# Kernel optimization log

Measured on AMD Instinct MI355X. Metric: run time of the kernel, lower is better.

The kernel has to match this reference:

```python
import jax, jax.numpy as jnp
import numpy as np

N_HEADS = 8
NUM_CLASSES = 8
ATTN_INTENSE = 1.0


def setup_inputs() -> dict:
    key = jax.random.key(0)
    k1, k2, k3, k4 = jax.random.split(key, 4)
    bs, width, T = 8, 1536, 1024
    qkv = jax.random.normal(k1, (bs, width, T), dtype=jnp.float32)
    attn_mask = jax.random.randint(k2, (bs, 32, 32), 0, NUM_CLASSES, dtype=jnp.int32)
    # class embedding table: NUM_CLASSES rows + 1 null row (used for the global pass)
    embed_table = jax.random.normal(k3, (NUM_CLASSES + 1, 512), dtype=jnp.float32) * 0.02
    # Conv1d(embed_dim=512 -> 3*ch=192, kernel=1, bias=False) weight
    W_cls = jax.random.normal(k4, (192, 512), dtype=jnp.float32) * 0.02
    return {"qkv": qkv, "attn_mask": attn_mask, "embed_table": embed_table, "W_cls": W_cls}


def _attend(q, k, v, scale):
    # q,k,v: [B, T, C]; returns [B, T, C]
    logits = jnp.einsum('btc,bsc->bts', q * scale, k * scale)
    w = jax.nn.softmax(logits, axis=-1)
    return jnp.einsum('bts,bsc->btc', w, v)


def reference(qkv, attn_mask, embed_table, W_cls):
    bs, width, T = qkv.shape
    H = N_HEADS
    ch = width // (3 * H)            # 64
    scale = ch ** -0.25              # 1/sqrt(sqrt(ch))
    bH = bs * H

    qkv_h = qkv.reshape(bH, 3 * ch, T)
    q = jnp.transpose(qkv_h[:, 0 * ch:1 * ch], (0, 2, 1))  # [bH, T, ch]
    k = jnp.transpose(qkv_h[:, 1 * ch:2 * ch], (0, 2, 1))
    v = jnp.transpose(qkv_h[:, 2 * ch:3 * ch], (0, 2, 1))

    # ---- global pass with null class token ----
    null_tok = W_cls @ embed_table[NUM_CLASSES]  # [3*ch]
    qn, kn, vn = null_tok[:ch], null_tok[ch:2 * ch], null_tok[2 * ch:]
    a = _attend(q + qn, k + kn, v + vn, scale)   # [bH, T, ch]

    # ---- per-region (per segmentation class) attention ----
    seg = attn_mask.reshape(bs, T)
    segs = jnp.repeat(seg, H, axis=0)            # [bH, T], sample-major like qkv reshape

    out = a
    counter = jnp.ones((bH, T), dtype=qkv.dtype)
    for c in range(NUM_CLASSES):
        tok = W_cls @ embed_table[c]             # [3*ch], same token at every region position
        qc, kc, vc = tok[:ch], tok[ch:2 * ch], tok[2 * ch:]
        m = segs == c                            # [bH, T]
        logits = jnp.einsum('btc,bsc->bts', (q + qc) * scale, (k + kc) * scale)
        logits = jnp.where(m[:, None, :], logits, -1e9)   # restrict keys to region
        w = jax.nn.softmax(logits, axis=-1)
        a_c = jnp.einsum('bts,bsc->btc', w, v + vc)
        out = out + jnp.where(m[:, :, None], a_c, 0.0)    # scatter-add onto region queries
        counter = counter + ATTN_INTENSE * m.astype(counter.dtype)

    out = out / counter[:, :, None]              # [bH, T, ch]
    # faithful to original: outs are [ch, T] each, torch.stack(dim=1) -> [ch, bH, T], then reshape
    stacked = jnp.transpose(out, (2, 0, 1))      # [ch, bH, T]
    return stacked.reshape(bs, H * ch, T)
```

## Files before the change

kernel.cpp:

```cpp
#include <hip/hip_runtime.h>
#include <stdint.h>

typedef unsigned short u16;
typedef unsigned int   u32;
typedef __bf16 bf16_t;
typedef bf16_t bf16x8 __attribute__((ext_vector_type(8)));
typedef bf16_t bf16x2 __attribute__((ext_vector_type(2)));
typedef float  f32x2  __attribute__((ext_vector_type(2)));
typedef float  f32x4  __attribute__((ext_vector_type(4)));

#define QSCALE 0.18033688011112042f

__device__ __forceinline__ u32 pkbf(float a, float b) {
  f32x2 x = {a, b};
  bf16x2 y = __builtin_convertvector(x, bf16x2);
  union { bf16x2 v; u32 u; } c; c.v = y; return c.u;
}

__device__ __forceinline__ float fexp2(float x) {
#if __has_builtin(__builtin_amdgcn_exp2f)
  return __builtin_amdgcn_exp2f(x);
#else
  float r;
  asm("v_exp_f32 %0, %1\n\ts_nop 0" : "=v"(r) : "v"(x));
  return r;
#endif
}

__device__ __forceinline__ void gload_lds16(const void* g, void* l) {
  __builtin_amdgcn_global_load_lds(
      (const __attribute__((address_space(1))) void*)g,
      (__attribute__((address_space(3))) void*)l, 16, 0, 0);
}

__global__ __launch_bounds__(256)
void prep_kernel(const float* __restrict__ qkv,
                 const float* __restrict__ W, const float* __restrict__ E,
                 float* __restrict__ tok, u16* __restrict__ tiles) {
  const int B = blockIdx.x;
  const int tid = threadIdx.x;
  if (B >= 1024) {
    const int gw = (B - 1024) * 4 + (tid >> 6);
    const int lane = tid & 63;
    if (gw < 1728) {
      const int c = gw / 192, j = gw - c * 192;
      const f32x4* w4 = (const f32x4*)(W + (size_t)j * 512 + lane * 8);
      const f32x4* e4 = (const f32x4*)(E + (size_t)c * 512 + lane * 8);
      float acc = 0.f;
#pragma unroll
      for (int i = 0; i < 2; ++i) {
        f32x4 w = w4[i], e = e4[i];
        acc += w.x * e.x + w.y * e.y + w.z * e.z + w.w * e.w;
      }
#pragma unroll
      for (int off = 32; off; off >>= 1) acc += __shfl_xor(acc, off, 64);
      if (lane == 0) tok[c * 192 + j] = acc;
    }
    return;
  }
  const int bh = B >> 4, kt = B & 15;
  const int s0 = kt * 64;
  const float* qg = qkv + (size_t)bh * 192 * 1024;
  u16* img = tiles + (size_t)B * 8192;
  {
    const int s = tid & 63, g = tid >> 6;
    const float* kb = qg + (size_t)(64 + g * 16) * 1024 + s0 + s;
    float kf[16];
#pragma unroll
    for (int i = 0; i < 16; ++i) kf[i] = kb[(size_t)i * 1024];
    u32 kp[8];
#pragma unroll
    for (int j2 = 0; j2 < 8; ++j2) kp[j2] = pkbf(kf[2 * j2], kf[2 * j2 + 1]);
    const int xr = (s & 7) << 3;
    *(uint4*)&img[s * 64 + ((g * 16)     ^ xr)] = make_uint4(kp[0], kp[1], kp[2], kp[3]);
    *(uint4*)&img[s * 64 + ((g * 16 + 8) ^ xr)] = make_uint4(kp[4], kp[5], kp[6], kp[7]);
  }
  {
    const int lV = tid & 15, dg = tid >> 4;
    const float* vb = qg + (size_t)(128 + dg * 4) * 1024 + s0 + lV;
#pragma unroll
    for (int i = 0; i < 4; ++i) {
      float v0 = vb[(size_t)i * 1024 +  0];
      float v1 = vb[(size_t)i * 1024 + 16];
      float v2 = vb[(size_t)i * 1024 + 32];
      float v3 = vb[(size_t)i * 1024 + 48];
      const int d = dg * 4 + i;
      *(uint2*)&img[4096 + d * 64 + ((lV * 4) ^ ((d & 7) << 3))] =
          make_uint2(pkbf(v0, v1), pkbf(v2, v3));
    }
  }
}

__global__ __launch_bounds__(256, 3)
void attn_kernel(const float* __restrict__ qkv, const int* __restrict__ seg,
                 const float* __restrict__ tok, const u16* __restrict__ tiles,
                 float* __restrict__ out) {
  __shared__ __align__(16) u16 smem[24576];

  const int L  = blockIdx.x;
  const int bh = (L & 7) * 8 + ((L >> 3) & 7);
  const int qt = L >> 6;
  const int b  = bh >> 3;
  const int tid = threadIdx.x, wave = tid >> 6, lane = tid & 63;
  const int quad = lane >> 4, l16 = lane & 15;
  u16* Pw = smem + 16384 + wave * 2048;

  const float* qg   = qkv + (size_t)bh * 192 * 1024;
  const int*   segb = seg + b * 1024;
  const u16*   tbh  = tiles + (size_t)bh * (16 * 8192);

  const int tq = qt * 64 + wave * 16 + l16;
  const int mycls = segb[tq];
  int sq[4];
#pragma unroll
  for (int r = 0; r < 4; ++r) sq[r] = segb[qt * 64 + wave * 16 + quad * 4 + r];

  const float* tn = tok + 8 * 192;
  const float* tc = tok + mycls * 192;
  union { u32 w[4]; bf16x8 v; } q0f[2], qbf[2];
#pragma unroll
  for (int kc = 0; kc < 2; ++kc)
#pragma unroll
    for (int jj = 0; jj < 4; ++jj) {
      int d = kc * 32 + quad * 8 + jj * 2;
      float a0 = qg[(size_t)d * 1024 + tq];
      float a1 = qg[(size_t)(d + 1) * 1024 + tq];
      q0f[kc].w[jj] = pkbf((a0 + tn[d]) * QSCALE, (a1 + tn[d + 1]) * QSCALE);
      qbf[kc].w[jj] = pkbf((a0 + tc[d]) * QSCALE, (a1 + tc[d + 1]) * QSCALE);
    }

  f32x4 O0[4], Ob[4];
#pragma unroll
  for (int dt = 0; dt < 4; ++dt) {
    O0[dt] = (f32x4){0.f, 0.f, 0.f, 0.f};
    Ob[dt] = (f32x4){0.f, 0.f, 0.f, 0.f};
  }
  float rs0[4] = {0.f, 0.f, 0.f, 0.f}, rsb[4] = {0.f, 0.f, 0.f, 0.f};

  {
    const char* src = (const char*)tbh + tid * 16;
    char* dst = (char*)smem + tid * 16;
#pragma unroll
    for (int i = 0; i < 4; ++i) gload_lds16(src + i * 4096, dst + i * 4096);
  }

  const int xq = (l16 & 7) << 3;

#pragma unroll 2
  for (int kt = 0; kt < 16; ++kt) {
    const int s0 = kt * 64;
    __syncthreads();
    if (kt + 1 < 16) {
      const char* src = (const char*)tbh + (size_t)(kt + 1) * 16384 + tid * 16;
      char* dst = (char*)smem + ((kt + 1) & 1) * 16384 + tid * 16;
#pragma unroll
      for (int i = 0; i < 4; ++i) gload_lds16(src + i * 4096, dst + i * 4096);
    }
    int sk[4];
#pragma unroll
    for (int n4 = 0; n4 < 4; ++n4) sk[n4] = segb[s0 + n4 * 16 + l16];

    const u16* ktr = smem + (kt & 1) * 8192;
    const u16* vls = ktr + 4096;

    f32x4 S0[4], Sb[4];
#pragma unroll
    for (int n4 = 0; n4 < 4; ++n4) {
      const int scol = n4 * 16 + l16;
      f32x4 a0 = {0.f, 0.f, 0.f, 0.f}, ab = {0.f, 0.f, 0.f, 0.f};
#pragma unroll
      for (int kc = 0; kc < 2; ++kc) {
        bf16x8 kfr = *(const bf16x8*)&ktr[scol * 64 + ((kc * 32 + quad * 8) ^ xq)];
        a0 = __builtin_amdgcn_mfma_f32_16x16x32_bf16(q0f[kc].v, kfr, a0, 0, 0, 0);
        ab = __builtin_amdgcn_mfma_f32_16x16x32_bf16(qbf[kc].v, kfr, ab, 0, 0, 0);
      }
      S0[n4] = a0; Sb[n4] = ab;
    }

#pragma unroll
    for (int r = 0; r < 4; ++r) {
      const int row = quad * 4 + r;
      const int po = row * 64 + ((l16 * 4) ^ ((row & 7) << 3));
      float p0[4], pb[4];
#pragma unroll
      for (int n4 = 0; n4 < 4; ++n4) {
        p0[n4] = fexp2(S0[n4][r]);
        pb[n4] = (sk[n4] == sq[r]) ? fexp2(Sb[n4][r]) : 0.f;
      }
      rs0[r] += (p0[0] + p0[1]) + (p0[2] + p0[3]);
      rsb[r] += (pb[0] + pb[1]) + (pb[2] + pb[3]);
      *(uint2*)&Pw[po]        = make_uint2(pkbf(p0[0], p0[1]), pkbf(p0[2], p0[3]));
      *(uint2*)&Pw[1024 + po] = make_uint2(pkbf(pb[0], pb[1]), pkbf(pb[2], pb[3]));
    }
    asm volatile("s_waitcnt lgkmcnt(0)" ::: "memory");

#pragma unroll
    for (int kc = 0; kc < 2; ++kc) {
      const int co = (kc * 32 + quad * 8) ^ xq;
      bf16x8 pf0 = *(const bf16x8*)&Pw[l16 * 64 + co];
      bf16x8 pfb = *(const bf16x8*)&Pw[1024 + l16 * 64 + co];
#pragma unroll
      for (int dt = 0; dt < 4; ++dt) {
        bf16x8 vfr = *(const bf16x8*)&vls[(dt * 16 + l16) * 64 + co];
        O0[dt] = __builtin_amdgcn_mfma_f32_16x16x32_bf16(pf0, vfr, O0[dt], 0, 0, 0);
        Ob[dt] = __builtin_amdgcn_mfma_f32_16x16x32_bf16(pfb, vfr, Ob[dt], 0, 0, 0);
      }
    }
  }

#pragma unroll
  for (int r = 0; r < 4; ++r)
#pragma unroll
    for (int off = 1; off < 16; off <<= 1) {
      rs0[r] += __shfl_xor(rs0[r], off, 64);
      rsb[r] += __shfl_xor(rsb[r], off, 64);
    }
  float inv0[4], invb[4];
#pragma unroll
  for (int r = 0; r < 4; ++r) {
    inv0[r] = (rs0[r] > 0.f) ? 1.f / rs0[r] : 0.f;
    invb[r] = (rsb[r] > 0.f) ? 1.f / rsb[r] : 0.f;
  }

  __syncthreads();
  float* fbuf = (float*)smem;
  const float* tvn = tok + 8 * 192 + 128;
#pragma unroll
  for (int dt = 0; dt < 4; ++dt) {
    const int d = dt * 16 + l16;
    const float bn = tvn[d];
#pragma unroll
    for (int r = 0; r < 4; ++r) {
      float bc = tok[sq[r] * 192 + 128 + d];
      float vA = O0[dt][r] * inv0[r] + bn;
      float vB = Ob[dt][r] * invb[r] + bc;
      fbuf[d * 65 + wave * 16 + quad * 4 + r] = 0.5f * (vA + vB);
    }
  }
  __syncthreads();
  {
    const size_t obase = (size_t)bh * 1024 + qt * 64;
    for (int i = tid; i < 4096; i += 256) {
      int d = i >> 6, t = i & 63;
      out[(size_t)d * 65536 + obase + t] = fbuf[d * 65 + t];
    }
  }
}

extern "C" void kernel_launch(void* const* d_in, const int* in_sizes, int n_in,
                              void* d_out, int out_size, void* d_ws, size_t ws_size,
                              hipStream_t stream) {
  (void)in_sizes; (void)n_in; (void)out_size; (void)ws_size;
  const float* qkv   = (const float*)d_in[0];
  const int*   amask = (const int*)d_in[1];
  const float* emb   = (const float*)d_in[2];
  const float* wcls  = (const float*)d_in[3];
  float* tok   = (float*)d_ws;
  u16*   tiles = (u16*)((char*)d_ws + 8192);
  float* out = (float*)d_out;

  hipLaunchKernelGGL(prep_kernel, dim3(1456), dim3(256), 0, stream,
                     qkv, wcls, emb, tok, tiles);
  hipLaunchKernelGGL(attn_kernel, dim3(1024), dim3(256), 0, stream,
                     qkv, amask, tok, tiles, out);
}
```

Measured before the change: 141.2 us.

## Compute transposed scores to keep P in registers, dropping the LDS round trip

```diff
diff --git a/kernel.cpp b/kernel.cpp
--- a/kernel.cpp
+++ b/kernel.cpp
@@ -76,26 +76,24 @@
     *(uint4*)&img[s * 64 + ((g * 16 + 8) ^ xr)] = make_uint4(kp[4], kp[5], kp[6], kp[7]);
   }
   {
-    const int lV = tid & 15, dg = tid >> 4;
-    const float* vb = qg + (size_t)(128 + dg * 4) * 1024 + s0 + lV;
+    const int g = tid & 15, dg = tid >> 4;
+    const int cp = ((g >> 3) & 1) * 32 + (g & 3) * 8 + ((g >> 2) & 1) * 4;
+    const float* vb = qg + (size_t)(128 + dg * 4) * 1024 + s0 + g * 4;
 #pragma unroll
     for (int i = 0; i < 4; ++i) {
-      float v0 = vb[(size_t)i * 1024 +  0];
-      float v1 = vb[(size_t)i * 1024 + 16];
-      float v2 = vb[(size_t)i * 1024 + 32];
-      float v3 = vb[(size_t)i * 1024 + 48];
+      f32x4 v = *(const f32x4*)(vb + (size_t)i * 1024);
       const int d = dg * 4 + i;
-      *(uint2*)&img[4096 + d * 64 + ((lV * 4) ^ ((d & 7) << 3))] =
-          make_uint2(pkbf(v0, v1), pkbf(v2, v3));
-    }
-  }
-}
-
-__global__ __launch_bounds__(256, 3)
+      *(uint2*)&img[4096 + d * 64 + (cp ^ ((d & 7) << 3))] =
+          make_uint2(pkbf(v.x, v.y), pkbf(v.z, v.w));
+    }
+  }
+}
+
+__global__ __launch_bounds__(256, 4)
 void attn_kernel(const float* __restrict__ qkv, const int* __restrict__ seg,
                  const float* __restrict__ tok, const u16* __restrict__ tiles,
                  float* __restrict__ out) {
-  __shared__ __align__(16) u16 smem[24576];
+  __shared__ __align__(16) u16 smem[16384];
 
   const int L  = blockIdx.x;
   const int bh = (L & 7) * 8 + ((L >> 3) & 7);
@@ -103,7 +101,6 @@
   const int b  = bh >> 3;
   const int tid = threadIdx.x, wave = tid >> 6, lane = tid & 63;
   const int quad = lane >> 4, l16 = lane & 15;
-  u16* Pw = smem + 16384 + wave * 2048;
 
   const float* qg   = qkv + (size_t)bh * 192 * 1024;
   const int*   segb = seg + b * 1024;
@@ -135,7 +132,7 @@
     O0[dt] = (f32x4){0.f, 0.f, 0.f, 0.f};
     Ob[dt] = (f32x4){0.f, 0.f, 0.f, 0.f};
   }
-  float rs0[4] = {0.f, 0.f, 0.f, 0.f}, rsb[4] = {0.f, 0.f, 0.f, 0.f};
+  float rs0 = 0.f, rsb = 0.f;
 
   {
     const char* src = (const char*)tbh + tid * 16;
@@ -156,70 +153,77 @@
 #pragma unroll
       for (int i = 0; i < 4; ++i) gload_lds16(src + i * 4096, dst + i * 4096);
     }
-    int sk[4];
-#pragma unroll
-    for (int n4 = 0; n4 < 4; ++n4) sk[n4] = segb[s0 + n4 * 16 + l16];
+    int sk[4][4];
+#pragma unroll
+    for (int n4 = 0; n4 < 4; ++n4) {
+      int4 s4 = *(const int4*)&segb[s0 + n4 * 16 + quad * 4];
+      sk[n4][0] = s4.x; sk[n4][1] = s4.y; sk[n4][2] = s4.z; sk[n4][3] = s4.w;
+    }
 
     const u16* ktr = smem + (kt & 1) * 8192;
     const u16* vls = ktr + 4096;
 
-    f32x4 S0[4], Sb[4];
+    f32x4 S0t[4], Sbt[4];
 #pragma unroll
     for (int n4 = 0; n4 < 4; ++n4) {
-      const int scol = n4 * 16 + l16;
+      const int srow = n4 * 16 + l16;
       f32x4 a0 = {0.f, 0.f, 0.f, 0.f}, ab = {0.f, 0.f, 0.f, 0.f};
 #pragma unroll
       for (int kc = 0; kc < 2; ++kc) {
-        bf16x8 kfr = *(const bf16x8*)&ktr[scol * 64 + ((kc * 32 + quad * 8) ^ xq)];
-        a0 = __builtin_amdgcn_mfma_f32_16x16x32_bf16(q0f[kc].v, kfr, a0, 0, 0, 0);
-        ab = __builtin_amdgcn_mfma_f32_16x16x32_bf16(qbf[kc].v, kfr, ab, 0, 0, 0);
-      }
-      S0[n4] = a0; Sb[n4] = ab;
-    }
-
-#pragma unroll
-    for (int r = 0; r < 4; ++r) {
-      const int row = quad * 4 + r;
-      const int po = row * 64 + ((l16 * 4) ^ ((row & 7) << 3));
-      float p0[4], pb[4];
-#pragma unroll
-      for (int n4 = 0; n4 < 4; ++n4) {
-        p0[n4] = fexp2(S0[n4][r]);
-        pb[n4] = (sk[n4] == sq[r]) ? fexp2(Sb[n4][r]) : 0.f;
-      }
-      rs0[r] += (p0[0] + p0[1]) + (p0[2] + p0[3]);
-      rsb[r] += (pb[0] + pb[1]) + (pb[2] + pb[3]);
-      *(uint2*)&Pw[po]        = make_uint2(pkbf(p0[0], p0[1]), pkbf(p0[2], p0[3]));
-      *(uint2*)&Pw[1024 + po] = make_uint2(pkbf(pb[0], pb[1]), pkbf(pb[2], pb[3]));
-    }
-    asm volatile("s_waitcnt lgkmcnt(0)" ::: "memory");
+        bf16x8 kfr = *(const bf16x8*)&ktr[srow * 64 + ((kc * 32 + quad * 8) ^ xq)];
+        a0 = __builtin_amdgcn_mfma_f32_16x16x32_bf16(kfr, q0f[kc].v, a0, 0, 0, 0);
+        ab = __builtin_amdgcn_mfma_f32_16x16x32_bf16(kfr, qbf[kc].v, ab, 0, 0, 0);
+      }
+      S0t[n4] = a0; Sbt[n4] = ab;
+    }
+
+    float p0[4][4], pb[4][4];
+#pragma unroll
+    for (int n4 = 0; n4 < 4; ++n4)
+#pragma unroll
+      for (int r = 0; r < 4; ++r) {
+        p0[n4][r] = fexp2(S0t[n4][r]);
+        pb[n4][r] = (sk[n4][r] == mycls) ? fexp2(Sbt[n4][r]) : 0.f;
+      }
+#pragma unroll
+    for (int n4 = 0; n4 < 4; ++n4) {
+      rs0 += (p0[n4][0] + p0[n4][1]) + (p0[n4][2] + p0[n4][3]);
+      rsb += (pb[n4][0] + pb[n4][1]) + (pb[n4][2] + pb[n4][3]);
+    }
+    union { u32 w[4]; bf16x8 v; } pa0[2], pab[2];
+#pragma unroll
+    for (int kc = 0; kc < 2; ++kc) {
+      pa0[kc].w[0] = pkbf(p0[2 * kc][0],     p0[2 * kc][1]);
+      pa0[kc].w[1] = pkbf(p0[2 * kc][2],     p0[2 * kc][3]);
+      pa0[kc].w[2] = pkbf(p0[2 * kc + 1][0], p0[2 * kc + 1][1]);
+      pa0[kc].w[3] = pkbf(p0[2 * kc + 1][2], p0[2 * kc + 1][3]);
+      pab[kc].w[0] = pkbf(pb[2 * kc][0],     pb[2 * kc][1]);
+      pab[kc].w[1] = pkbf(pb[2 * kc][2],     pb[2 * kc][3]);
+      pab[kc].w[2] = pkbf(pb[2 * kc + 1][0], pb[2 * kc + 1][1]);
+      pab[kc].w[3] = pkbf(pb[2 * kc + 1][2], pb[2 * kc + 1][3]);
+    }
 
 #pragma unroll
     for (int kc = 0; kc < 2; ++kc) {
       const int co = (kc * 32 + quad * 8) ^ xq;
-      bf16x8 pf0 = *(const bf16x8*)&Pw[l16 * 64 + co];
-      bf16x8 pfb = *(const bf16x8*)&Pw[1024 + l16 * 64 + co];
 #pragma unroll
       for (int dt = 0; dt < 4; ++dt) {
         bf16x8 vfr = *(const bf16x8*)&vls[(dt * 16 + l16) * 64 + co];
-        O0[dt] = __builtin_amdgcn_mfma_f32_16x16x32_bf16(pf0, vfr, O0[dt], 0, 0, 0);
-        Ob[dt] = __builtin_amdgcn_mfma_f32_16x16x32_bf16(pfb, vfr, Ob[dt], 0, 0, 0);
-      }
-    }
-  }
-
-#pragma unroll
-  for (int r = 0; r < 4; ++r)
-#pragma unroll
-    for (int off = 1; off < 16; off <<= 1) {
-      rs0[r] += __shfl_xor(rs0[r], off, 64);
-      rsb[r] += __shfl_xor(rsb[r], off, 64);
-    }
+        O0[dt] = __builtin_amdgcn_mfma_f32_16x16x32_bf16(pa0[kc].v, vfr, O0[dt], 0, 0, 0);
+        Ob[dt] = __builtin_amdgcn_mfma_f32_16x16x32_bf16(pab[kc].v, vfr, Ob[dt], 0, 0, 0);
+      }
+    }
+  }
+
+  rs0 += __shfl_xor(rs0, 16, 64);  rs0 += __shfl_xor(rs0, 32, 64);
+  rsb += __shfl_xor(rsb, 16, 64);  rsb += __shfl_xor(rsb, 32, 64);
   float inv0[4], invb[4];
 #pragma unroll
   for (int r = 0; r < 4; ++r) {
-    inv0[r] = (rs0[r] > 0.f) ? 1.f / rs0[r] : 0.f;
-    invb[r] = (rsb[r] > 0.f) ? 1.f / rsb[r] : 0.f;
+    float d0 = __shfl(rs0, quad * 4 + r, 16);
+    float db = __shfl(rsb, quad * 4 + r, 16);
+    inv0[r] = (d0 > 0.f) ? 1.f / d0 : 0.f;
+    invb[r] = (db > 0.f) ? 1.f / db : 0.f;
   }
 
   __syncthreads();
```

New measurement: 137.3 us. -2.8%, faster.
